# Optimization experiments

Hardware: AMD Instinct MI355X
Metric: run time of the kernel (lower is better)

Reference implementation:

```python
import jax, jax.numpy as jnp
import numpy as np

B, H, W, CIN, COUT = 4, 128, 128, 16, 16
FH, FW = 2 * H - 1, 2 * W - 1  # fft_shape = 2*k - 1 per spatial dim (SAME, stride 1)


def setup_inputs() -> dict:
    key = jax.random.key(0)
    k1, k2, k3, k4 = jax.random.split(key, 4)
    inputs = jax.random.normal(k1, (B, H, W, CIN), dtype=jnp.float32)
    # Fourier-space complex kernel, represented as two real arrays
    kernel_real = jax.random.normal(k2, (FH, FW, CIN, COUT), dtype=jnp.float32) * 0.05
    kernel_imag = jax.random.normal(k3, (FH, FW, CIN, COUT), dtype=jnp.float32) * 0.05
    bias = jax.random.normal(k4, (1, 1, 1, COUT), dtype=jnp.float32) * 0.01
    return {"inputs": inputs, "kernel_real": kernel_real, "kernel_imag": kernel_imag, "bias": bias}


def reference(inputs, kernel_real, kernel_imag, bias):
    kernel = kernel_real + 1j * kernel_imag  # (FH, FW, CIN, COUT) complex64
    b, h, w, cin = inputs.shape
    fft_shape = (2 * h - 1, 2 * w - 1)
    # FFT over spatial dims, zero-padded to fft_shape -> (B, FH, FW, CIN) complex64
    y = jnp.fft.fftn(inputs, axes=(1, 2), s=fft_shape)
    # Broadcast complex multiply + inverse FFT: (B, FH, FW, CIN, COUT)
    y = jnp.fft.ifftn(y[..., None] * kernel, axes=(1, 2)).real
    # 'SAME' slice: center crop back to the input spatial size
    sh = (fft_shape[0] - h) // 2
    sw = (fft_shape[1] - w) // 2
    y = y[:, sh:sh + h, sw:sw + w]  # (B, H, W, CIN, COUT)
    # Faithful to the source: sum over axis=-1 (the `features` axis), leaving CIN channels
    y = jnp.sum(y, axis=-1)  # (B, H, W, CIN)
    return y + bias  # bias broadcasts because COUT == CIN
```

## Files before the change

kernel.cpp:

```cpp
#include <hip/hip_runtime.h>
#include <math.h>


constexpr float PI2_OVER_N = 6.28318530717958647692f / 255.0f;
constexpr float INV_N2 = 1.0f / (255.0f * 255.0f);

typedef __attribute__((ext_vector_type(8))) short bf16x8;
typedef __attribute__((ext_vector_type(4))) float f32x4;
#define MFMA16 __builtin_amdgcn_mfma_f32_16x16x32_bf16

__device__ __forceinline__ int remap_bc(int xidx) {
  int k = xidx & 7, j = xidx >> 3;
  return ((k >> 1) * 16) + ((k & 1) * 8) + j;
}

__device__ __forceinline__ void cmul_update(float& tr, float& ti, float fr, float fi) {
  float ntr = tr * fr - ti * fi;
  ti = tr * fi + ti * fr;
  tr = ntr;
}

__device__ __forceinline__ unsigned short bf16h(float f) {
  unsigned u = __float_as_uint(f);
  return (unsigned short)((u + 0x7FFFu + ((u >> 16) & 1u)) >> 16);
}
__device__ __forceinline__ float bf16f(unsigned short h) {
  return __uint_as_float(((unsigned)h) << 16);
}


__device__ __forceinline__ void ksum_body(
    int buf, int xb, const float* __restrict__ kr, const float* __restrict__ ki,
    float* __restrict__ Sr, float* __restrict__ Si) {
  const int nrows = 255 * 255 * 16;
  int r = xb * 256 + threadIdx.x;
  if (r >= nrows) return;
  const float* src = (buf == 0) ? kr : ki;
  float* dst = (buf == 0) ? Sr : Si;
  const float4* k4 = (const float4*)(src + (size_t)r * 16);
  float4 a = k4[0], b = k4[1], c = k4[2], d = k4[3];
  dst[r] = a.x + a.y + a.z + a.w + b.x + b.y + b.z + b.w +
           c.x + c.y + c.z + c.w + d.x + d.y + d.z + d.w;
}

__device__ __forceinline__ void stage1_body(
    int cid, const float* __restrict__ x, float4* __restrict__ U4) {
  int bm = cid & 511;
  int yc = cid >> 9;
  int l = threadIdx.x & 63;
  int g = __builtin_amdgcn_readfirstlane(threadIdx.x >> 6);
  int c = yc * 4 + g;
  const float* xs = x + (size_t)bm * 2048 + c;
  float s0, c0, s1, c1;
  sincosf(PI2_OVER_N * (float)(2 * l), &s0, &c0);
  sincosf(PI2_OVER_N * (float)(2 * l + 1), &s1, &c1);
  float f0r = c0, f0i = -s0, f1r = c1, f1i = -s1;
  float t0r = 1.f, t0i = 0.f, t1r = 1.f, t1i = 0.f;
  float ar0 = 0.f, ai0 = 0.f, ar1 = 0.f, ai1 = 0.f;
#pragma unroll 4
  for (int n = 0; n < 128; ++n) {
    float xx = xs[n * 16];
    ar0 += xx * t0r; ai0 += xx * t0i;
    ar1 += xx * t1r; ai1 += xx * t1i;
    cmul_update(t0r, t0i, f0r, f0i);
    cmul_update(t1r, t1i, f1r, f1i);
  }
  int b = bm >> 7, m = bm & 127;
  U4[((size_t)(b * 16 + c) * 128 + m) * 64 + l] = make_float4(ar0, ai0, ar1, ai1);
}

__device__ __forceinline__ void build_body(
    int cid2, short* __restrict__ t2, short* __restrict__ t4, short* __restrict__ t5) {
  int i = cid2 * 256 + threadIdx.x;
  float s, c;
  if (i < 196608) {
    int plane = i >> 15;
    int r = i & 32767;
    int pt = r >> 11, r2 = r & 2047;
    int moct = r2 >> 7, p = (r2 >> 3) & 15, j = r2 & 7;
    int pg = pt * 16 + p, m = moct * 8 + j;
    int k = ((pg % 255) * m) % 255;
    sincosf(PI2_OVER_N * (float)k, &s, &c);
    float ti = -s;
    float src = (plane < 2) ? c : ((plane < 4) ? ti : -ti);
    unsigned short h = bf16h(src);
    t2[i] = (short)((plane & 1) ? bf16h(src - bf16f(h)) : h);
  } else if (i < 393216) {
    int i2 = i - 196608;
    int plane = i2 >> 15;
    int r = i2 & 32767;
    int ht = r >> 12, r2 = r & 4095;
    int poct = r2 >> 7, h = (r2 >> 3) & 15, j = r2 & 7;
    int p = poct * 8 + j;
    unsigned short val = 0;
    if (p < 255) {
      int hg = ht * 16 + h;
      int k = ((hg + 63) * p) % 255;
      sincosf(PI2_OVER_N * (float)k, &s, &c);
      float src = (plane < 2) ? c : ((plane < 4) ? s : -s);
      unsigned short hh = bf16h(src);
      val = (plane & 1) ? bf16h(src - bf16f(hh)) : hh;
    }
    t4[i2] = (short)val;
  } else {
    int i3 = i - 393216;
    int plane = i3 >> 15;
    int r = i3 & 32767;
    int wt = r >> 12, r2 = r & 4095;
    int ko = r2 >> 7, wl = (r2 >> 3) & 15, j = r2 & 7;
    int q = (ko * 8 + j) & 127;
    int ww = wt * 16 + wl;
    sincosf(PI2_OVER_N * (float)(((ww + 63) * q) % 255), &s, &c);
    float src = (plane < 2) ? c : -s;
    unsigned short hh = bf16h(src);
    t5[i3] = (short)((plane & 1) ? bf16h(src - bf16f(hh)) : hh);
  }
}

__global__ __launch_bounds__(256) void fused_front(
    const float* __restrict__ kr, const float* __restrict__ ki,
    float* __restrict__ Sr, float* __restrict__ Si,
    const float* __restrict__ x, float4* __restrict__ U4,
    short* __restrict__ t2, short* __restrict__ t4, short* __restrict__ t5) {
  int bid = blockIdx.x;
  int d3 = bid / 3, r3 = bid - d3 * 3;
  if (r3 == 2) {
    int cid = d3;
    if (cid < 2048) stage1_body(cid, x, U4);
    else            build_body(cid - 2048, t2, t4, t5);
  } else {
    int kid = d3 * 2 + r3;
    ksum_body(kid & 1, kid >> 1, kr, ki, Sr, Si);
  }
}

__global__ __launch_bounds__(256) void fold(
    const float* __restrict__ Sr, const float* __restrict__ Si,
    float2* __restrict__ keff2) {
  int p = blockIdx.x;
  int q = blockIdx.y * 16 + (threadIdx.x >> 4);
  int c = threadIdx.x & 15;
  int pp = (255 - p) % 255;
  int qq = (255 - q) % 255;
  size_t i0 = (size_t)(p * 255 + q) * 16 + c;
  size_t i1 = (size_t)(pp * 255 + qq) * 16 + c;
  float sr0 = Sr[i0], si0 = Si[i0], sr1 = Sr[i1], si1 = Si[i1];
  float2 v;
  v.x = 0.5f * (sr0 + sr1);
  v.y = 0.5f * (si0 - si1);
  keff2[((size_t)c * 255 + p) * 128 + q] = v;
}

__global__ __launch_bounds__(256) void pack_u(
    const float4* __restrict__ U4, short* __restrict__ ub) {
  int bc = remap_bc(blockIdx.x);
  int mo = blockIdx.y * 2 + (threadIdx.x >> 7);
  int q = threadIdx.x & 127;
  float r[8], im[8];
#pragma unroll
  for (int j = 0; j < 8; ++j) {
    float4 u = U4[((size_t)bc * 128 + mo * 8 + j) * 64 + (q >> 1)];
    r[j]  = (q & 1) ? u.z : u.x;
    im[j] = (q & 1) ? u.w : u.y;
  }
  unsigned short hr[8], lr[8], hi_[8], li[8];
#pragma unroll
  for (int j = 0; j < 8; ++j) {
    hr[j] = bf16h(r[j]);   lr[j] = bf16h(r[j] - bf16f(hr[j]));
    hi_[j] = bf16h(im[j]); li[j] = bf16h(im[j] - bf16f(hi_[j]));
  }
  size_t base = (size_t)bc * 65536 + (size_t)(q >> 4) * 2048 + (size_t)mo * 128 + (size_t)(q & 15) * 8;
  const unsigned short* planes[4] = {hr, lr, hi_, li};
#pragma unroll
  for (int pl = 0; pl < 4; ++pl) {
    const unsigned short* v = planes[pl];
    uint4 o;
    o.x = (unsigned)v[0] | ((unsigned)v[1] << 16);
    o.y = (unsigned)v[2] | ((unsigned)v[3] << 16);
    o.z = (unsigned)v[4] | ((unsigned)v[5] << 16);
    o.w = (unsigned)v[6] | ((unsigned)v[7] << 16);
    *(uint4*)(ub + base + (size_t)pl * 16384) = o;
  }
}

__global__ __launch_bounds__(256) void stage2_mfma(
    const short* __restrict__ ub, const short* __restrict__ t2,
    const float2* __restrict__ keff2, short* __restrict__ zb) {
  int bc = remap_bc(blockIdx.x);
  int c = bc & 15;
  int w = threadIdx.x >> 6;
  int lane = threadIdx.x & 63;
  int quad = lane >> 4, col = lane & 15;
  int pt = blockIdx.y;
  int qh = w;
  f32x4 accr[2] = {{0,0,0,0},{0,0,0,0}};
  f32x4 acci[2] = {{0,0,0,0},{0,0,0,0}};
  const short* ubase = ub + (size_t)bc * 65536;
#pragma unroll
  for (int ko = 0; ko < 4; ++ko) {
    int moct = ko * 4 + quad;
    const short* ta = t2 + ((size_t)(pt * 16 + moct) * 16 + col) * 8;
    bf16x8 arh = *(const bf16x8*)(ta);
    bf16x8 arl = *(const bf16x8*)(ta + 32768);
    bf16x8 aih = *(const bf16x8*)(ta + 2 * 32768);
    bf16x8 ail = *(const bf16x8*)(ta + 3 * 32768);
    bf16x8 anh = *(const bf16x8*)(ta + 4 * 32768);
    bf16x8 anl = *(const bf16x8*)(ta + 5 * 32768);
#pragma unroll
    for (int qq = 0; qq < 2; ++qq) {
      int qt = qh * 2 + qq;
      const short* tb = ubase + ((size_t)(qt * 16 + moct) * 16 + col) * 8;
      bf16x8 brh = *(const bf16x8*)(tb);
      bf16x8 brl = *(const bf16x8*)(tb + 16384);
      bf16x8 bih = *(const bf16x8*)(tb + 2 * 16384);
      bf16x8 bil = *(const bf16x8*)(tb + 3 * 16384);
      accr[qq] = MFMA16(arh, brh, accr[qq], 0, 0, 0);
      accr[qq] = MFMA16(arh, brl, accr[qq], 0, 0, 0);
      accr[qq] = MFMA16(arl, brh, accr[qq], 0, 0, 0);
      accr[qq] = MFMA16(anh, bih, accr[qq], 0, 0, 0);
      accr[qq] = MFMA16(anh, bil, accr[qq], 0, 0, 0);
      accr[qq] = MFMA16(anl, bih, accr[qq], 0, 0, 0);
      acci[qq] = MFMA16(arh, bih, acci[qq], 0, 0, 0);
      acci[qq] = MFMA16(arh, bil, acci[qq], 0, 0, 0);
      acci[qq] = MFMA16(arl, bih, acci[qq], 0, 0, 0);
      acci[qq] = MFMA16(aih, brh, acci[qq], 0, 0, 0);
      acci[qq] = MFMA16(aih, brl, acci[qq], 0, 0, 0);
      acci[qq] = MFMA16(ail, brh, acci[qq], 0, 0, 0);
    }
  }
  int poct = pt * 2 + (quad >> 1);
  size_t joff = (size_t)col * 8 + (quad & 1) * 4;
#pragma unroll
  for (int qq = 0; qq < 2; ++qq) {
    int qt = qh * 2 + qq;
    int qg = qt * 16 + col;
    float zr[4], zi[4];
#pragma unroll
    for (int r = 0; r < 4; ++r) {
      int pg = pt * 16 + quad * 4 + r;
      int pgc = pg < 255 ? pg : 254;
      float2 k = keff2[((size_t)c * 255 + pgc) * 128 + qg];
      float xr = accr[qq][r], xi = acci[qq][r];
      zr[r] = k.x * xr - k.y * xi;
      zi[r] = k.x * xi + k.y * xr;
    }
    unsigned short hr[4], lr[4], hi_[4], li[4];
#pragma unroll
    for (int r = 0; r < 4; ++r) {
      hr[r] = bf16h(zr[r]);  lr[r] = bf16h(zr[r] - bf16f(hr[r]));
      hi_[r] = bf16h(zi[r]); li[r] = bf16h(zi[r] - bf16f(hi_[r]));
    }
    size_t base = (size_t)bc * 131072 + (size_t)qt * 4096 + (size_t)poct * 128 + joff;
    uint2 o;
    o.x = (unsigned)hr[0] | ((unsigned)hr[1] << 16);
    o.y = (unsigned)hr[2] | ((unsigned)hr[3] << 16);
    *(uint2*)(zb + base) = o;
    o.x = (unsigned)lr[0] | ((unsigned)lr[1] << 16);
    o.y = (unsigned)lr[2] | ((unsigned)lr[3] << 16);
    *(uint2*)(zb + base + 32768) = o;
    o.x = (unsigned)hi_[0] | ((unsigned)hi_[1] << 16);
    o.y = (unsigned)hi_[2] | ((unsigned)hi_[3] << 16);
    *(uint2*)(zb + base + 2 * 32768) = o;
    o.x = (unsigned)li[0] | ((unsigned)li[1] << 16);
    o.y = (unsigned)li[2] | ((unsigned)li[3] << 16);
    *(uint2*)(zb + base + 3 * 32768) = o;
  }
}

__global__ __launch_bounds__(256) void stage4_mfma(
    const short* __restrict__ zb, const short* __restrict__ t4,
    short* __restrict__ a5, float* __restrict__ v0) {
  int bc = remap_bc(blockIdx.x);
  int w = threadIdx.x >> 6;
  int lane = threadIdx.x & 63;
  int quad = lane >> 4, col = lane & 15;
  int u = blockIdx.y * 4 + w;
  int qt = u >> 3;
  int kseg = (u >> 2) & 1;
  int htp = u & 3;
  f32x4 accr[2] = {{0,0,0,0},{0,0,0,0}};
  f32x4 acci[2] = {{0,0,0,0},{0,0,0,0}};
  const short* zbase = zb + (size_t)bc * 131072;
#pragma unroll
  for (int ko = 0; ko < 4; ++ko) {
    int poct = kseg * 16 + ko * 4 + quad;
    const short* tz = zbase + ((size_t)(qt * 32 + poct) * 16 + col) * 8;
    bf16x8 zrh = *(const bf16x8*)(tz);
    bf16x8 zrl = *(const bf16x8*)(tz + 32768);
    bf16x8 zih = *(const bf16x8*)(tz + 2 * 32768);
    bf16x8 zil = *(const bf16x8*)(tz + 3 * 32768);
#pragma unroll
    for (int t = 0; t < 2; ++t) {
      int ht = htp * 2 + t;
      const short* ta = t4 + ((size_t)(ht * 32 + poct) * 16 + col) * 8;
      bf16x8 trh = *(const bf16x8*)(ta);
      bf16x8 trl = *(const bf16x8*)(ta + 32768);
      bf16x8 tih = *(const bf16x8*)(ta + 2 * 32768);
      bf16x8 til = *(const bf16x8*)(ta + 3 * 32768);
      bf16x8 tnh = *(const bf16x8*)(ta + 4 * 32768);
      bf16x8 tnl = *(const bf16x8*)(ta + 5 * 32768);
      accr[t] = MFMA16(zrh, trh, accr[t], 0, 0, 0);
      accr[t] = MFMA16(zrh, trl, accr[t], 0, 0, 0);
      accr[t] = MFMA16(zrl, trh, accr[t], 0, 0, 0);
      accr[t] = MFMA16(zih, tnh, accr[t], 0, 0, 0);
      accr[t] = MFMA16(zih, tnl, accr[t], 0, 0, 0);
      accr[t] = MFMA16(zil, tnh, accr[t], 0, 0, 0);
      acci[t] = MFMA16(zih, trh, acci[t], 0, 0, 0);
      acci[t] = MFMA16(zih, trl, acci[t], 0, 0, 0);
      acci[t] = MFMA16(zil, trh, acci[t], 0, 0, 0);
      acci[t] = MFMA16(zrh, tih, acci[t], 0, 0, 0);
      acci[t] = MFMA16(zrh, til, acci[t], 0, 0, 0);
      acci[t] = MFMA16(zrl, tih, acci[t], 0, 0, 0);
    }
  }
  int ko_s = kseg * 16 + qt * 2 + (quad >> 1);
  int j0 = (quad & 1) * 4;
#pragma unroll
  for (int t = 0; t < 2; ++t) {
    int ht = htp * 2 + t;
    unsigned short vh[4], vl[4], wh[4], wl2[4];
#pragma unroll
    for (int r = 0; r < 4; ++r) {
      vh[r] = bf16h(accr[t][r]);  vl[r] = bf16h(accr[t][r] - bf16f(vh[r]));
      wh[r] = bf16h(acci[t][r]);  wl2[r] = bf16h(acci[t][r] - bf16f(wh[r]));
    }
    size_t base = (((size_t)(bc * 4) * 8 + ht) * 32 + ko_s) * 128 + (size_t)col * 8 + j0;
    uint2 o;
    o.x = (unsigned)vh[0] | ((unsigned)vh[1] << 16);
    o.y = (unsigned)vh[2] | ((unsigned)vh[3] << 16);
    *(uint2*)(a5 + base) = o;
    o.x = (unsigned)vl[0] | ((unsigned)vl[1] << 16);
    o.y = (unsigned)vl[2] | ((unsigned)vl[3] << 16);
    *(uint2*)(a5 + base + 32768) = o;
    o.x = (unsigned)wh[0] | ((unsigned)wh[1] << 16);
    o.y = (unsigned)wh[2] | ((unsigned)wh[3] << 16);
    *(uint2*)(a5 + base + 2 * 32768) = o;
    o.x = (unsigned)wl2[0] | ((unsigned)wl2[1] << 16);
    o.y = (unsigned)wl2[2] | ((unsigned)wl2[3] << 16);
    *(uint2*)(a5 + base + 3 * 32768) = o;
    if (qt == 0 && quad == 0)
      v0[(size_t)(kseg * 64 + bc) * 128 + ht * 16 + col] = accr[t][0];
  }
}

__global__ __launch_bounds__(256) void stage5_mfma(
    const short* __restrict__ a5, const short* __restrict__ t5,
    const float* __restrict__ v0, const float* __restrict__ bias,
    float* __restrict__ out) {
  int bc = remap_bc(blockIdx.x);
  int w = threadIdx.x >> 6;
  int lane = threadIdx.x & 63;
  int quad = lane >> 4, col = lane & 15;
  int u = blockIdx.y * 4 + w;
  int ht = u >> 2;
  int wtp = u & 3;
  f32x4 acc[2] = {{0,0,0,0},{0,0,0,0}};
  const short* abase = a5 + (size_t)bc * 131072;
#pragma unroll
  for (int kc = 0; kc < 8; ++kc) {
    int koq = kc * 4 + quad;
    const short* pa = abase + ((size_t)(ht * 32 + koq) * 16 + col) * 8;
    bf16x8 vrh = *(const bf16x8*)(pa);
    bf16x8 vrl = *(const bf16x8*)(pa + 32768);
    bf16x8 vih = *(const bf16x8*)(pa + 2 * 32768);
    bf16x8 vil = *(const bf16x8*)(pa + 3 * 32768);
#pragma unroll
    for (int t = 0; t < 2; ++t) {
      int wt = wtp * 2 + t;
      const short* pb = t5 + ((size_t)(wt * 32 + koq) * 16 + col) * 8;
      bf16x8 tch = *(const bf16x8*)(pb);
      bf16x8 tcl = *(const bf16x8*)(pb + 32768);
      bf16x8 tnh = *(const bf16x8*)(pb + 2 * 32768);
      bf16x8 tnl = *(const bf16x8*)(pb + 3 * 32768);
      acc[t] = MFMA16(vrh, tch, acc[t], 0, 0, 0);
      acc[t] = MFMA16(vrh, tcl, acc[t], 0, 0, 0);
      acc[t] = MFMA16(vrl, tch, acc[t], 0, 0, 0);
      acc[t] = MFMA16(vih, tnh, acc[t], 0, 0, 0);
      acc[t] = MFMA16(vih, tnl, acc[t], 0, 0, 0);
      acc[t] = MFMA16(vil, tnh, acc[t], 0, 0, 0);
    }
  }
  int b = bc >> 4, c = bc & 15;
  float bb = bias[c];
  float v0t[4];
#pragma unroll
  for (int r = 0; r < 4; ++r) {
    int h = ht * 16 + quad * 4 + r;
    v0t[r] = v0[(size_t)bc * 128 + h] + v0[(size_t)(64 + bc) * 128 + h];
  }
#pragma unroll
  for (int t = 0; t < 2; ++t) {
    int ww = (wtp * 2 + t) * 16 + col;
#pragma unroll
    for (int r = 0; r < 4; ++r) {
      int h = ht * 16 + quad * 4 + r;
      out[((size_t)(b * 128 + h) * 128 + ww) * 16 + c] =
          (2.0f * acc[t][r] - v0t[r]) * INV_N2 + bb;
    }
  }
}

extern "C" void kernel_launch(void* const* d_in, const int* in_sizes, int n_in,
                              void* d_out, int out_size, void* d_ws, size_t ws_size,
                              hipStream_t stream) {
  const float* x  = (const float*)d_in[0];
  const float* kr = (const float*)d_in[1];
  const float* ki = (const float*)d_in[2];
  const float* bs = (const float*)d_in[3];
  float* out = (float*)d_out;

  char* p = (char*)d_ws;
  float2* keff2 = (float2*)p; p += (size_t)16 * 255 * 128 * 8;
  short*  zb    = (short*)p;  p += (size_t)64 * 131072 * 2;
  float4* U4    = (float4*)p;
  short*  a5    = (short*)p;  p += (size_t)64 * 131072 * 2;
  short*  ub    = (short*)p;  p += (size_t)64 * 65536 * 2;
  short*  t2    = (short*)p;  p += (size_t)196608 * 2;
  short*  t4    = (short*)p;  p += (size_t)196608 * 2;
  short*  t5    = (short*)p;  p += (size_t)131072 * 2;
  float*  v0    = (float*)p;  p += (size_t)2 * 64 * 128 * 4;
  float* Sr = (float*)zb;
  float* Si = Sr + 255 * 255 * 16;

  fused_front<<<12288, 256, 0, stream>>>(kr, ki, Sr, Si, x, U4, t2, t4, t5);
  fold<<<dim3(255, 8), 256, 0, stream>>>(Sr, Si, keff2);
  pack_u<<<dim3(64, 8), 256, 0, stream>>>(U4, ub);
  stage2_mfma<<<dim3(64, 16), 256, 0, stream>>>(ub, t2, keff2, zb);
  stage4_mfma<<<dim3(64, 16), 256, 0, stream>>>(zb, t4, a5, v0);
  stage5_mfma<<<dim3(64, 8), 256, 0, stream>>>(a5, t5, v0, bs, out);
}
```

Before: 218.7 us.

## Move first-axis DFT to split-bf16 MFMA and fuse fold with it

Replaces the scalar twiddle-recurrence stage-1 DFT with a split-bf16 (hi/lo) MFMA matmul against a precomputed twiddle table t1. The front kernel now packs x into bf16 hi/lo planes and builds t1. The old fold and pack_u kernels are merged into one 'mid' kernel that interleaves fold blocks with the MFMA stage-1 blocks, which write ub directly. This drops a launch and the fp32 U4 round trip, but adds x packing and twiddle-table building work, and bf16-split precision becomes a factor.

Result: faster. 208.4 us (-4.7%).

```diff
diff --git a/kernel.cpp b/kernel.cpp
--- a/kernel.cpp
+++ b/kernel.cpp
@@ -12,12 +12,6 @@
 __device__ __forceinline__ int remap_bc(int xidx) {
   int k = xidx & 7, j = xidx >> 3;
   return ((k >> 1) * 16) + ((k & 1) * 8) + j;
-}
-
-__device__ __forceinline__ void cmul_update(float& tr, float& ti, float fr, float fi) {
-  float ntr = tr * fr - ti * fi;
-  ti = tr * fi + ti * fr;
-  tr = ntr;
 }
 
 __device__ __forceinline__ unsigned short bf16h(float f) {
@@ -43,33 +37,50 @@
            c.x + c.y + c.z + c.w + d.x + d.y + d.z + d.w;
 }
 
-__device__ __forceinline__ void stage1_body(
-    int cid, const float* __restrict__ x, float4* __restrict__ U4) {
-  int bm = cid & 511;
-  int yc = cid >> 9;
-  int l = threadIdx.x & 63;
-  int g = __builtin_amdgcn_readfirstlane(threadIdx.x >> 6);
-  int c = yc * 4 + g;
-  const float* xs = x + (size_t)bm * 2048 + c;
-  float s0, c0, s1, c1;
-  sincosf(PI2_OVER_N * (float)(2 * l), &s0, &c0);
-  sincosf(PI2_OVER_N * (float)(2 * l + 1), &s1, &c1);
-  float f0r = c0, f0i = -s0, f1r = c1, f1i = -s1;
-  float t0r = 1.f, t0i = 0.f, t1r = 1.f, t1i = 0.f;
-  float ar0 = 0.f, ai0 = 0.f, ar1 = 0.f, ai1 = 0.f;
-#pragma unroll 4
-  for (int n = 0; n < 128; ++n) {
-    float xx = xs[n * 16];
-    ar0 += xx * t0r; ai0 += xx * t0i;
-    ar1 += xx * t1r; ai1 += xx * t1i;
-    cmul_update(t0r, t0i, f0r, f0i);
-    cmul_update(t1r, t1i, f1r, f1i);
-  }
-  int b = bm >> 7, m = bm & 127;
-  U4[((size_t)(b * 16 + c) * 128 + m) * 64 + l] = make_float4(ar0, ai0, ar1, ai1);
-}
-
-__device__ __forceinline__ void build_body(
+__device__ __forceinline__ void packx_body(
+    int pid, const float* __restrict__ x, short* __restrict__ xp) {
+  int bc = pid & 63;
+  int mt = pid >> 6;
+  int b = bc >> 4, c = bc & 15;
+  int mcol = threadIdx.x & 15;
+  int noct = threadIdx.x >> 4;
+  int m = mt * 16 + mcol;
+  const float* xs = x + ((size_t)(b * 128 + m) * 128 + noct * 8) * 16 + c;
+  unsigned short hi[8], lo[8];
+#pragma unroll
+  for (int j = 0; j < 8; ++j) {
+    float v = xs[j * 16];
+    hi[j] = bf16h(v);
+    lo[j] = bf16h(v - bf16f(hi[j]));
+  }
+  size_t base = (size_t)bc * 32768 + ((size_t)(mt * 16 + noct) * 16 + mcol) * 8;
+  uint4 o;
+  o.x = (unsigned)hi[0] | ((unsigned)hi[1] << 16);
+  o.y = (unsigned)hi[2] | ((unsigned)hi[3] << 16);
+  o.z = (unsigned)hi[4] | ((unsigned)hi[5] << 16);
+  o.w = (unsigned)hi[6] | ((unsigned)hi[7] << 16);
+  *(uint4*)(xp + base) = o;
+  o.x = (unsigned)lo[0] | ((unsigned)lo[1] << 16);
+  o.y = (unsigned)lo[2] | ((unsigned)lo[3] << 16);
+  o.z = (unsigned)lo[4] | ((unsigned)lo[5] << 16);
+  o.w = (unsigned)lo[6] | ((unsigned)lo[7] << 16);
+  *(uint4*)(xp + base + 16384) = o;
+}
+
+__device__ __forceinline__ void buildt1_body(int cid, short* __restrict__ t1) {
+  int i = cid * 256 + threadIdx.x;
+  int plane = i >> 14;
+  int r = i & 16383;
+  int qt = r >> 11, noct = (r >> 7) & 15, qcol = (r >> 3) & 15, j = r & 7;
+  int q = qt * 16 + qcol, n = noct * 8 + j;
+  float s, c;
+  sincosf(PI2_OVER_N * (float)((q * n) % 255), &s, &c);
+  float src = (plane < 2) ? c : -s;
+  unsigned short hh = bf16h(src);
+  t1[i] = (short)((plane & 1) ? bf16h(src - bf16f(hh)) : hh);
+}
+
+__device__ __forceinline__ void buildt24_body(
     int cid2, short* __restrict__ t2, short* __restrict__ t4, short* __restrict__ t5) {
   int i = cid2 * 256 + threadIdx.x;
   float s, c;
@@ -120,25 +131,28 @@
 __global__ __launch_bounds__(256) void fused_front(
     const float* __restrict__ kr, const float* __restrict__ ki,
     float* __restrict__ Sr, float* __restrict__ Si,
-    const float* __restrict__ x, float4* __restrict__ U4,
-    short* __restrict__ t2, short* __restrict__ t4, short* __restrict__ t5) {
+    const float* __restrict__ x, short* __restrict__ xp,
+    short* __restrict__ t1, short* __restrict__ t2,
+    short* __restrict__ t4, short* __restrict__ t5) {
   int bid = blockIdx.x;
-  int d3 = bid / 3, r3 = bid - d3 * 3;
-  if (r3 == 2) {
-    int cid = d3;
-    if (cid < 2048) stage1_body(cid, x, U4);
-    else            build_body(cid - 2048, t2, t4, t5);
+  int d = bid >> 2, r = bid & 3;
+  if (r == 3) {
+    if (d < 512)      packx_body(d, x, xp);
+    else if (d < 768) buildt1_body(d - 512, t1);
+    else              buildt24_body(d - 768, t2, t4, t5);
   } else {
-    int kid = d3 * 2 + r3;
-    ksum_body(kid & 1, kid >> 1, kr, ki, Sr, Si);
-  }
-}
-
-__global__ __launch_bounds__(256) void fold(
-    const float* __restrict__ Sr, const float* __restrict__ Si,
+    int kid = d * 3 + r;
+    if (kid < 8192) ksum_body(kid & 1, kid >> 1, kr, ki, Sr, Si);
+  }
+}
+
+
+__device__ __forceinline__ void fold_body(
+    int fid, const float* __restrict__ Sr, const float* __restrict__ Si,
     float2* __restrict__ keff2) {
-  int p = blockIdx.x;
-  int q = blockIdx.y * 16 + (threadIdx.x >> 4);
+  int p = fid % 255;
+  int qy = fid / 255;
+  int q = qy * 16 + (threadIdx.x >> 4);
   int c = threadIdx.x & 15;
   int pp = (255 - p) % 255;
   int qq = (255 - q) % 255;
@@ -151,35 +165,82 @@
   keff2[((size_t)c * 255 + p) * 128 + q] = v;
 }
 
-__global__ __launch_bounds__(256) void pack_u(
-    const float4* __restrict__ U4, short* __restrict__ ub) {
-  int bc = remap_bc(blockIdx.x);
-  int mo = blockIdx.y * 2 + (threadIdx.x >> 7);
-  int q = threadIdx.x & 127;
-  float r[8], im[8];
-#pragma unroll
-  for (int j = 0; j < 8; ++j) {
-    float4 u = U4[((size_t)bc * 128 + mo * 8 + j) * 64 + (q >> 1)];
-    r[j]  = (q & 1) ? u.z : u.x;
-    im[j] = (q & 1) ? u.w : u.y;
-  }
-  unsigned short hr[8], lr[8], hi_[8], li[8];
-#pragma unroll
-  for (int j = 0; j < 8; ++j) {
-    hr[j] = bf16h(r[j]);   lr[j] = bf16h(r[j] - bf16f(hr[j]));
-    hi_[j] = bf16h(im[j]); li[j] = bf16h(im[j] - bf16f(hi_[j]));
-  }
-  size_t base = (size_t)bc * 65536 + (size_t)(q >> 4) * 2048 + (size_t)mo * 128 + (size_t)(q & 15) * 8;
-  const unsigned short* planes[4] = {hr, lr, hi_, li};
-#pragma unroll
-  for (int pl = 0; pl < 4; ++pl) {
-    const unsigned short* v = planes[pl];
-    uint4 o;
-    o.x = (unsigned)v[0] | ((unsigned)v[1] << 16);
-    o.y = (unsigned)v[2] | ((unsigned)v[3] << 16);
-    o.z = (unsigned)v[4] | ((unsigned)v[5] << 16);
-    o.w = (unsigned)v[6] | ((unsigned)v[7] << 16);
-    *(uint4*)(ub + base + (size_t)pl * 16384) = o;
+__device__ __forceinline__ void s1g_body(
+    int gid, const short* __restrict__ xp, const short* __restrict__ t1,
+    short* __restrict__ ub) {
+  int bc = gid & 63;
+  int mt = gid >> 6;
+  int w = threadIdx.x >> 6;
+  int lane = threadIdx.x & 63;
+  int quad = lane >> 4, col = lane & 15;
+  f32x4 ur[2] = {{0,0,0,0},{0,0,0,0}};
+  f32x4 ui[2] = {{0,0,0,0},{0,0,0,0}};
+  const short* xb = xp + (size_t)bc * 32768;
+#pragma unroll
+  for (int ko = 0; ko < 4; ++ko) {
+    int noct = ko * 4 + quad;
+    const short* pa = xb + ((size_t)(mt * 16 + noct) * 16 + col) * 8;
+    bf16x8 xh = *(const bf16x8*)(pa);
+    bf16x8 xl = *(const bf16x8*)(pa + 16384);
+#pragma unroll
+    for (int qq = 0; qq < 2; ++qq) {
+      int qt = w * 2 + qq;
+      const short* pb = t1 + ((size_t)(qt * 16 + noct) * 16 + col) * 8;
+      bf16x8 ch = *(const bf16x8*)(pb);
+      bf16x8 cl = *(const bf16x8*)(pb + 16384);
+      bf16x8 nh = *(const bf16x8*)(pb + 2 * 16384);
+      bf16x8 nl = *(const bf16x8*)(pb + 3 * 16384);
+      ur[qq] = MFMA16(xh, ch, ur[qq], 0, 0, 0);
+      ur[qq] = MFMA16(xh, cl, ur[qq], 0, 0, 0);
+      ur[qq] = MFMA16(xl, ch, ur[qq], 0, 0, 0);
+      ur[qq] = MFMA16(xl, cl, ur[qq], 0, 0, 0);
+      ui[qq] = MFMA16(xh, nh, ui[qq], 0, 0, 0);
+      ui[qq] = MFMA16(xh, nl, ui[qq], 0, 0, 0);
+      ui[qq] = MFMA16(xl, nh, ui[qq], 0, 0, 0);
+      ui[qq] = MFMA16(xl, nl, ui[qq], 0, 0, 0);
+    }
+  }
+  int moct = mt * 2 + (quad >> 1);
+  int j0 = (quad & 1) * 4;
+#pragma unroll
+  for (int qq = 0; qq < 2; ++qq) {
+    int qt = w * 2 + qq;
+    unsigned short rh[4], rl[4], ih[4], il[4];
+#pragma unroll
+    for (int r = 0; r < 4; ++r) {
+      rh[r] = bf16h(ur[qq][r]); rl[r] = bf16h(ur[qq][r] - bf16f(rh[r]));
+      ih[r] = bf16h(ui[qq][r]); il[r] = bf16h(ui[qq][r] - bf16f(ih[r]));
+    }
+    size_t base = (size_t)bc * 65536 + (size_t)qt * 2048 + (size_t)moct * 128 +
+                  (size_t)col * 8 + j0;
+    uint2 o;
+    o.x = (unsigned)rh[0] | ((unsigned)rh[1] << 16);
+    o.y = (unsigned)rh[2] | ((unsigned)rh[3] << 16);
+    *(uint2*)(ub + base) = o;
+    o.x = (unsigned)rl[0] | ((unsigned)rl[1] << 16);
+    o.y = (unsigned)rl[2] | ((unsigned)rl[3] << 16);
+    *(uint2*)(ub + base + 16384) = o;
+    o.x = (unsigned)ih[0] | ((unsigned)ih[1] << 16);
+    o.y = (unsigned)ih[2] | ((unsigned)ih[3] << 16);
+    *(uint2*)(ub + base + 2 * 16384) = o;
+    o.x = (unsigned)il[0] | ((unsigned)il[1] << 16);
+    o.y = (unsigned)il[2] | ((unsigned)il[3] << 16);
+    *(uint2*)(ub + base + 3 * 16384) = o;
+  }
+}
+
+__global__ __launch_bounds__(256) void mid(
+    const float* __restrict__ Sr, const float* __restrict__ Si,
+    float2* __restrict__ keff2,
+    const short* __restrict__ xp, const short* __restrict__ t1,
+    short* __restrict__ ub) {
+  int bid = blockIdx.x;
+  int d = bid / 5, r = bid - d * 5;
+  if (r == 4) {
+    s1g_body(d, xp, t1, ub);
+  } else {
+    int fid = d * 4 + r;
+    if (fid < 2040) fold_body(fid, Sr, Si, keff2);
   }
 }
 
@@ -412,7 +473,7 @@
   char* p = (char*)d_ws;
   float2* keff2 = (float2*)p; p += (size_t)16 * 255 * 128 * 8;
   short*  zb    = (short*)p;  p += (size_t)64 * 131072 * 2;
-  float4* U4    = (float4*)p;
+  char*   a5reg = p;
   short*  a5    = (short*)p;  p += (size_t)64 * 131072 * 2;
   short*  ub    = (short*)p;  p += (size_t)64 * 65536 * 2;
   short*  t2    = (short*)p;  p += (size_t)196608 * 2;
@@ -421,10 +482,11 @@
   float*  v0    = (float*)p;  p += (size_t)2 * 64 * 128 * 4;
   float* Sr = (float*)zb;
   float* Si = Sr + 255 * 255 * 16;
-
-  fused_front<<<12288, 256, 0, stream>>>(kr, ki, Sr, Si, x, U4, t2, t4, t5);
-  fold<<<dim3(255, 8), 256, 0, stream>>>(Sr, Si, keff2);
-  pack_u<<<dim3(64, 8), 256, 0, stream>>>(U4, ub);
+  short* xp = (short*)a5reg;
+  short* t1 = (short*)(a5reg + 6 * 1024 * 1024);
+
+  fused_front<<<11264, 256, 0, stream>>>(kr, ki, Sr, Si, x, xp, t1, t2, t4, t5);
+  mid<<<2560, 256, 0, stream>>>(Sr, Si, keff2, xp, t1, ub);
   stage2_mfma<<<dim3(64, 16), 256, 0, stream>>>(ub, t2, keff2, zb);
   stage4_mfma<<<dim3(64, 16), 256, 0, stream>>>(zb, t4, a5, v0);
   stage5_mfma<<<dim3(64, 8), 256, 0, stream>>>(a5, t5, v0, bs, out);
```
